# Kernel optimization log

Measured on AMD Instinct MI355X. Metric: run time of the kernel, lower is better.

## Reference

```python
import jax, jax.numpy as jnp
import numpy as np

# config constants (from init_kwargs)
MAX_WORD_LENGTH = 8
RESIDUAL_THRESHOLD = 1e-3
DECAY_FACTOR = 0.9


def setup_inputs() -> dict:
    key = jax.random.key(0)
    k1, k2 = jax.random.split(key)
    targets = jax.random.normal(k1, (8192, 1024), dtype=jnp.float32)
    codebook = jax.random.normal(k2, (4096, 1024), dtype=jnp.float32)
    return {"targets": targets, "codebook": codebook}


def reference(targets, codebook):
    """Batched greedy residual pursuit.

    targets:  [B, D] semantic vectors
    codebook: [K, D] syllable vectors
    Returns (indices [B, L] int32 with -1 where the per-sample loop broke,
             final residual [B, D]).
    """
    B = targets.shape[0]

    def step(carry, s):
        residual, active = carry  # [B, D], [B] bool
        # break condition checked BEFORE selecting, as in the torch loop
        norm = jnp.sqrt(jnp.sum(residual * residual, axis=-1))  # [B]
        active = active & (norm >= RESIDUAL_THRESHOLD)
        scores = jnp.einsum("bd,kd->bk", residual, codebook)  # [B, K]
        idx = jnp.argmax(scores, axis=-1)  # [B]
        decay = jnp.power(jnp.float32(DECAY_FACTOR), s.astype(jnp.float32))
        contribution = decay * codebook[idx]  # [B, D]
        residual = jnp.where(active[:, None], residual - contribution, residual)
        out_idx = jnp.where(active, idx, -1).astype(jnp.int32)
        return (residual, active), out_idx

    init = (targets, jnp.ones((B,), dtype=bool))
    (residual, _), idx_seq = jax.lax.scan(step, init, jnp.arange(MAX_WORD_LENGTH))
    indices = jnp.transpose(idx_seq)  # [B, L]
    return indices, residual
```

## Files before the change

### kernel.cpp

```cpp
#include <hip/hip_runtime.h>
#include <hip/hip_bf16.h>
#include <math.h>

#define NB 8192
#define NK 4096
#define ND 1024
#define NL 8
#define RES_THR 1e-3f

typedef __bf16 bf16x8 __attribute__((ext_vector_type(8)));
typedef float f32x4 __attribute__((ext_vector_type(4)));

#define MFMA16(a, b, c) __builtin_amdgcn_mfma_f32_16x16x32_bf16(a, b, c, 0, 0, 0)

#define GLOAD(g, l)                                                        \
  __builtin_amdgcn_global_load_lds(                                        \
      (const __attribute__((address_space(1))) void*)(g),                  \
      (__attribute__((address_space(3))) void*)(l), 16, 0, 0)

__device__ __forceinline__ unsigned short f2bf(float x) {
  __hip_bfloat16 h = __float2bfloat16(x);
  return __builtin_bit_cast(unsigned short, h);
}
__device__ __forceinline__ float bf2f(unsigned short u) {
  return __bfloat162float(__builtin_bit_cast(__hip_bfloat16, u));
}

__device__ __forceinline__ float wave_reduce_sum(float v) {
#pragma unroll
  for (int off = 32; off > 0; off >>= 1) v += __shfl_down(v, off);
  return v;
}

__device__ __forceinline__ void top2_merge(float& v1, int& k1, float& v2,
                                           int& k2, float w1, int j1, float w2,
                                           int j2) {
  if (w1 > v1 || (w1 == v1 && j1 < k1)) {
    if (v1 > w2 || (v1 == w2 && k1 < j2)) { v2 = v1; k2 = k1; }
    else { v2 = w2; k2 = j2; }
    v1 = w1; k1 = j1;
  } else {
    if (w1 > v2 || (w1 == v2 && j1 < k2)) { v2 = w1; k2 = j1; }
  }
}

__global__ __launch_bounds__(256) void k_prep(const float* __restrict__ cb,
                                              unsigned short* __restrict__ Bh) {
  int b = blockIdx.x, t = threadIdx.x;
  float4 v = ((const float4*)(cb + (size_t)b * ND))[t];
  ushort4 h;
  h.x = f2bf(v.x); h.y = f2bf(v.y); h.z = f2bf(v.z); h.w = f2bf(v.w);
  ((ushort4*)(Bh + (size_t)b * ND))[t] = h;
}

__global__ __launch_bounds__(256) void k_init(const float* __restrict__ tgt,
                                              float* __restrict__ resid,
                                              unsigned short* __restrict__ Ah,
                                              int* __restrict__ active) {
  int b = blockIdx.x, t = threadIdx.x;
  float4 v = ((const float4*)(tgt + (size_t)b * ND))[t];
  ((float4*)(resid + (size_t)b * ND))[t] = v;
  ushort4 h;
  h.x = f2bf(v.x); h.y = f2bf(v.y); h.z = f2bf(v.z); h.w = f2bf(v.w);
  ((ushort4*)(Ah + (size_t)b * ND))[t] = h;
  float ss = v.x * v.x + v.y * v.y + v.z * v.z + v.w * v.w;
  ss = wave_reduce_sum(ss);
  __shared__ float red[4];
  if ((t & 63) == 0) red[t >> 6] = ss;
  __syncthreads();
  if (t == 0) {
    float tot = red[0] + red[1] + red[2] + red[3];
    active[b] = (sqrtf(tot) >= RES_THR) ? 1 : 0;
  }
}

__global__ __launch_bounds__(512) void k_score0(
    const unsigned short* __restrict__ Ah, const unsigned short* __restrict__ Bh,
    float4* __restrict__ part, unsigned short* __restrict__ sc) {
  __shared__ __align__(16) char sA0[32768];
  __shared__ __align__(16) char sA1[32768];
  __shared__ __align__(16) char sB0[32768];
  __shared__ __align__(16) char sB1[32768];
  const int tid = threadIdx.x;
  const int lane = tid & 63;
  const int swzid = (blockIdx.x & 7) * 64 + (blockIdx.x >> 3);
  const int bm = swzid >> 4;
  const int bn = swzid & 15;
  const int wid = tid >> 6;
  const int wr = wid >> 2;
  const int wc = wid & 3;

  const int srow = tid >> 3;
  const int sblk = (tid & 7) ^ (srow & 7);
  const unsigned short* aSrc = Ah + (size_t)(bm * 256 + srow) * ND + sblk * 8;
  const unsigned short* bSrc = Bh + (size_t)(bn * 256 + srow) * ND + sblk * 8;

  const int lr = lane & 15;
  const int lk = lane >> 4;
  const int swz = lr & 7;
  const int kb0 = ((lk ^ swz) << 4);
  const int kb1 = (((4 + lk) ^ swz) << 4);

  f32x4 acc[8][4];
#pragma unroll
  for (int m = 0; m < 8; ++m)
#pragma unroll
    for (int n = 0; n < 4; ++n) acc[m][n] = (f32x4)(0.f);

#pragma unroll
  for (int rr = 0; rr < 4; ++rr) {
    GLOAD(aSrc + (size_t)(rr * 64) * ND, sA0 + rr * 8192 + tid * 16);
    GLOAD(bSrc + (size_t)(rr * 64) * ND, sB0 + rr * 8192 + tid * 16);
  }
#pragma unroll
  for (int rr = 0; rr < 4; ++rr) {
    GLOAD(aSrc + (size_t)(rr * 64) * ND + 64, sA1 + rr * 8192 + tid * 16);
    GLOAD(bSrc + (size_t)(rr * 64) * ND + 64, sB1 + rr * 8192 + tid * 16);
  }

#pragma unroll 1
  for (int kt = 0; kt < 16; ++kt) {
    const char* pa = (kt & 1) ? sA1 : sA0;
    const char* pb = (kt & 1) ? sB1 : sB0;
    if (kt < 15) {
      asm volatile("s_waitcnt vmcnt(8)" ::: "memory");
    } else {
      asm volatile("s_waitcnt vmcnt(0)" ::: "memory");
    }
    __builtin_amdgcn_s_barrier();
    bf16x8 af0[8], bf0[4];
#pragma unroll
    for (int m = 0; m < 8; ++m)
      af0[m] = *(const bf16x8*)(pa + (wr * 128 + m * 16 + lr) * 128 + kb0);
#pragma unroll
    for (int n = 0; n < 4; ++n)
      bf0[n] = *(const bf16x8*)(pb + (wc * 64 + n * 16 + lr) * 128 + kb0);
    __builtin_amdgcn_s_setprio(1);
#pragma unroll
    for (int m = 0; m < 8; ++m)
#pragma unroll
      for (int n = 0; n < 4; ++n) acc[m][n] = MFMA16(af0[m], bf0[n], acc[m][n]);
    __builtin_amdgcn_s_setprio(0);
    bf16x8 af1[8], bf1[4];
#pragma unroll
    for (int m = 0; m < 8; ++m)
      af1[m] = *(const bf16x8*)(pa + (wr * 128 + m * 16 + lr) * 128 + kb1);
#pragma unroll
    for (int n = 0; n < 4; ++n)
      bf1[n] = *(const bf16x8*)(pb + (wc * 64 + n * 16 + lr) * 128 + kb1);
    __syncthreads();
    if (kt < 14) {
      const int k0 = (kt + 2) << 6;
      char* da = (kt & 1) ? sA1 : sA0;
      char* db = (kt & 1) ? sB1 : sB0;
#pragma unroll
      for (int rr = 0; rr < 4; ++rr) {
        GLOAD(aSrc + (size_t)(rr * 64) * ND + k0, da + rr * 8192 + tid * 16);
        GLOAD(bSrc + (size_t)(rr * 64) * ND + k0, db + rr * 8192 + tid * 16);
      }
    }
    __builtin_amdgcn_s_setprio(1);
#pragma unroll
    for (int m = 0; m < 8; ++m)
#pragma unroll
      for (int n = 0; n < 4; ++n) acc[m][n] = MFMA16(af1[m], bf1[n], acc[m][n]);
    __builtin_amdgcn_s_setprio(0);
  }
  __syncthreads();

  if (sc) {
#pragma unroll
    for (int m = 0; m < 8; ++m) {
      int row = bm * 256 + wr * 128 + m * 16 + lk * 4;
#pragma unroll
      for (int q = 0; q < 4; ++q)
#pragma unroll
        for (int n = 0; n < 4; ++n)
          sc[(size_t)(row + q) * NK + bn * 256 + wc * 64 + n * 16 + lr] =
              f2bf(acc[m][n][q]);
    }
  }

  if (part) {
    float4* red = (float4*)sA0;
#pragma unroll
    for (int m = 0; m < 8; ++m) {
#pragma unroll
      for (int q = 0; q < 4; ++q) {
        float v1 = acc[m][0][q];
        int k1 = bn * 256 + wc * 64 + lr;
        float v2 = -INFINITY;
        int k2 = 0x7fffffff;
#pragma unroll
        for (int n = 1; n < 4; ++n) {
          top2_merge(v1, k1, v2, k2, acc[m][n][q],
                     bn * 256 + wc * 64 + n * 16 + lr, -INFINITY, 0x7fffffff);
        }
#pragma unroll
        for (int msk = 1; msk < 16; msk <<= 1) {
          float ov1 = __shfl_xor(v1, msk);
          int ok1 = __shfl_xor(k1, msk);
          float ov2 = __shfl_xor(v2, msk);
          int ok2 = __shfl_xor(k2, msk);
          top2_merge(v1, k1, v2, k2, ov1, ok1, ov2, ok2);
        }
        if (lr == 0) {
          int row = wr * 128 + m * 16 + lk * 4 + q;
          red[row * 4 + wc] =
              make_float4(v1, __int_as_float(k1), v2, __int_as_float(k2));
        }
      }
    }
    __syncthreads();
    if (tid < 256) {
      float4 e0 = red[tid * 4 + 0];
      float v1 = e0.x; int k1 = __float_as_int(e0.y);
      float v2 = e0.z; int k2 = __float_as_int(e0.w);
#pragma unroll
      for (int j = 1; j < 4; ++j) {
        float4 e = red[tid * 4 + j];
        top2_merge(v1, k1, v2, k2, e.x, __float_as_int(e.y), e.z,
                   __float_as_int(e.w));
      }
      part[(size_t)(bm * 256 + tid) * 16 + bn] =
          make_float4(v1, __int_as_float(k1), v2, __int_as_float(k2));
    }
  }
}

__global__ __launch_bounds__(512) void k_gram(const unsigned short* __restrict__ Bh,
                                              unsigned short* __restrict__ G) {
  __shared__ __align__(16) char sA0[32768];
  __shared__ __align__(16) char sA1[32768];
  __shared__ __align__(16) char sB0[32768];
  __shared__ __align__(16) char sB1[32768];
  const int tid = threadIdx.x;
  const int lane = tid & 63;
  const int bm = blockIdx.x >> 4;
  const int bn = blockIdx.x & 15;
  const int wid = tid >> 6;
  const int wr = wid >> 2;
  const int wc = wid & 3;
  const int srow = tid >> 3;
  const int sblk = (tid & 7) ^ (srow & 7);
  const unsigned short* aSrc = Bh + (size_t)(bm * 256 + srow) * ND + sblk * 8;
  const unsigned short* bSrc = Bh + (size_t)(bn * 256 + srow) * ND + sblk * 8;
  const int lr = lane & 15;
  const int lk = lane >> 4;
  const int swz = lr & 7;
  const int kb0 = ((lk ^ swz) << 4);
  const int kb1 = (((4 + lk) ^ swz) << 4);

  f32x4 acc[8][4];
#pragma unroll
  for (int m = 0; m < 8; ++m)
#pragma unroll
    for (int n = 0; n < 4; ++n) acc[m][n] = (f32x4)(0.f);

#pragma unroll
  for (int rr = 0; rr < 4; ++rr) {
    GLOAD(aSrc + (size_t)(rr * 64) * ND, sA0 + rr * 8192 + tid * 16);
    GLOAD(bSrc + (size_t)(rr * 64) * ND, sB0 + rr * 8192 + tid * 16);
  }
#pragma unroll
  for (int rr = 0; rr < 4; ++rr) {
    GLOAD(aSrc + (size_t)(rr * 64) * ND + 64, sA1 + rr * 8192 + tid * 16);
    GLOAD(bSrc + (size_t)(rr * 64) * ND + 64, sB1 + rr * 8192 + tid * 16);
  }
#pragma unroll 1
  for (int kt = 0; kt < 16; ++kt) {
    const char* pa = (kt & 1) ? sA1 : sA0;
    const char* pb = (kt & 1) ? sB1 : sB0;
    if (kt < 15) {
      asm volatile("s_waitcnt vmcnt(8)" ::: "memory");
    } else {
      asm volatile("s_waitcnt vmcnt(0)" ::: "memory");
    }
    __builtin_amdgcn_s_barrier();
    bf16x8 af0[8], bf0[4];
#pragma unroll
    for (int m = 0; m < 8; ++m)
      af0[m] = *(const bf16x8*)(pa + (wr * 128 + m * 16 + lr) * 128 + kb0);
#pragma unroll
    for (int n = 0; n < 4; ++n)
      bf0[n] = *(const bf16x8*)(pb + (wc * 64 + n * 16 + lr) * 128 + kb0);
    __builtin_amdgcn_s_setprio(1);
#pragma unroll
    for (int m = 0; m < 8; ++m)
#pragma unroll
      for (int n = 0; n < 4; ++n) acc[m][n] = MFMA16(af0[m], bf0[n], acc[m][n]);
    __builtin_amdgcn_s_setprio(0);
    bf16x8 af1[8], bf1[4];
#pragma unroll
    for (int m = 0; m < 8; ++m)
      af1[m] = *(const bf16x8*)(pa + (wr * 128 + m * 16 + lr) * 128 + kb1);
#pragma unroll
    for (int n = 0; n < 4; ++n)
      bf1[n] = *(const bf16x8*)(pb + (wc * 64 + n * 16 + lr) * 128 + kb1);
    __syncthreads();
    if (kt < 14) {
      const int k0 = (kt + 2) << 6;
      char* da = (kt & 1) ? sA1 : sA0;
      char* db = (kt & 1) ? sB1 : sB0;
#pragma unroll
      for (int rr = 0; rr < 4; ++rr) {
        GLOAD(aSrc + (size_t)(rr * 64) * ND + k0, da + rr * 8192 + tid * 16);
        GLOAD(bSrc + (size_t)(rr * 64) * ND + k0, db + rr * 8192 + tid * 16);
      }
    }
    __builtin_amdgcn_s_setprio(1);
#pragma unroll
    for (int m = 0; m < 8; ++m)
#pragma unroll
      for (int n = 0; n < 4; ++n) acc[m][n] = MFMA16(af1[m], bf1[n], acc[m][n]);
    __builtin_amdgcn_s_setprio(0);
  }
#pragma unroll
  for (int m = 0; m < 8; ++m) {
    int row = bm * 256 + wr * 128 + m * 16 + lk * 4;
#pragma unroll
    for (int q = 0; q < 4; ++q)
#pragma unroll
      for (int n = 0; n < 4; ++n)
        G[(size_t)(row + q) * NK + bn * 256 + wc * 64 + n * 16 + lr] =
            f2bf(acc[m][n][q]);
  }
}

__global__ __launch_bounds__(256) void k_all(
    const unsigned short* __restrict__ sc0, const unsigned short* __restrict__ G,
    const float* __restrict__ cb, float* __restrict__ resid,
    float* __restrict__ out_idx, const int* __restrict__ active0) {
  const int b = blockIdx.x, t = threadIdx.x;
  __shared__ float s_max[4];
  __shared__ float s_nrm[4];
  __shared__ float s_red[4];
  __shared__ int s_cnt;
  __shared__ int s_spec;
  __shared__ int s_k[64];
  __shared__ float s_bv;
  __shared__ int s_bk;

  float4 r = ((const float4*)(resid + (size_t)b * ND))[t];

  float scv[16];
  {
    const unsigned short* srow = sc0 + (size_t)b * NK;
    uint4 v0 = *(const uint4*)(srow + t * 8);
    uint4 v1 = *(const uint4*)(srow + 2048 + t * 8);
    unsigned w[8] = {v0.x, v0.y, v0.z, v0.w, v1.x, v1.y, v1.z, v1.w};
#pragma unroll
    for (int j = 0; j < 8; ++j) {
      scv[2 * j] = bf2f((unsigned short)(w[j] & 0xffff));
      scv[2 * j + 1] = bf2f((unsigned short)(w[j] >> 16));
    }
  }
  int act = active0[b];
  float decay = 1.0f;

#pragma unroll 1
  for (int s = 0; s < NL; ++s) {
    float m = scv[0];
#pragma unroll
    for (int i = 1; i < 16; ++i) m = fmaxf(m, scv[i]);
    float ss = r.x * r.x + r.y * r.y + r.z * r.z + r.w * r.w;
#pragma unroll
    for (int off = 32; off > 0; off >>= 1) {
      m = fmaxf(m, __shfl_xor(m, off));
      ss += __shfl_xor(ss, off);
    }
    if ((t & 63) == 0) { s_max[t >> 6] = m; s_nrm[t >> 6] = ss; }
    if (t == 0) {
      s_cnt = 0;
      s_spec = 0x7fffffff;
      s_bv = -INFINITY;
      s_bk = 0x7fffffff;
    }
    __syncthreads();
    const float M = fmaxf(fmaxf(s_max[0], s_max[1]), fmaxf(s_max[2], s_max[3]));
    const float nrm = s_nrm[0] + s_nrm[1] + s_nrm[2] + s_nrm[3];
    act = (act && sqrtf(nrm) >= RES_THR) ? 1 : 0;
    const float margin = (s == 0) ? 2.5f : 6.0f;
#pragma unroll
    for (int i = 0; i < 16; ++i) {
      if (scv[i] >= M - margin) {
        int col = (i < 8) ? (t * 8 + i) : (2048 + t * 8 + (i - 8));
        int pos = atomicAdd(&s_cnt, 1);
        if (pos < 64) s_k[pos] = col;
        if (scv[i] == M) atomicMin(&s_spec, col);
      }
    }
    __syncthreads();
    const int cnt = s_cnt < 64 ? s_cnt : 64;
    int kbest;
    if (cnt <= 1) {
      kbest = s_spec;
    } else {
      for (int c = 0; c < cnt; ++c) {
        int k = s_k[c];
        float4 cv = ((const float4*)(cb + (size_t)k * ND))[t];
        float dd = r.x * cv.x + r.y * cv.y + r.z * cv.z + r.w * cv.w;
        dd = wave_reduce_sum(dd);
        if ((t & 63) == 0) s_red[t >> 6] = dd;
        __syncthreads();
        if (t == 0) {
          float scr = s_red[0] + s_red[1] + s_red[2] + s_red[3];
          if (scr > s_bv || (scr == s_bv && k < s_bk)) { s_bv = scr; s_bk = k; }
        }
        __syncthreads();
      }
      kbest = s_bk;
    }
    if (t == 0) out_idx[(size_t)b * NL + s] = act ? (float)kbest : -1.0f;
    if (act) {
      float4 cv = ((const float4*)(cb + (size_t)kbest * ND))[t];
      r.x -= decay * cv.x;
      r.y -= decay * cv.y;
      r.z -= decay * cv.z;
      r.w -= decay * cv.w;
      if (s < NL - 1) {
        const unsigned short* grow = G + (size_t)kbest * NK;
        uint4 g0 = *(const uint4*)(grow + t * 8);
        uint4 g1 = *(const uint4*)(grow + 2048 + t * 8);
        unsigned w[8] = {g0.x, g0.y, g0.z, g0.w, g1.x, g1.y, g1.z, g1.w};
#pragma unroll
        for (int j = 0; j < 8; ++j) {
          scv[2 * j] -= decay * bf2f((unsigned short)(w[j] & 0xffff));
          scv[2 * j + 1] -= decay * bf2f((unsigned short)(w[j] >> 16));
        }
      }
    }
    decay *= 0.9f;
    __syncthreads();
  }
  ((float4*)(resid + (size_t)b * ND))[t] = r;
}

__global__ __launch_bounds__(256) void k_update(
    float* __restrict__ resid, const float* __restrict__ cb,
    const float4* __restrict__ part, int* __restrict__ active,
    float* __restrict__ out_idx, unsigned short* __restrict__ Ah, float decay,
    int s, int nseg, float margin) {
  int b = blockIdx.x, t = threadIdx.x;
  __shared__ int s_cnt;
  __shared__ int s_k[32];
  __shared__ float s_red[4];
  __shared__ float s_bv;
  __shared__ int s_bk;

  float4 r = ((const float4*)(resid + (size_t)b * ND))[t];

  if (t < 2 * nseg) {
    float4 e = part[(size_t)b * 16 + (t >> 1)];
    float v = (t & 1) ? e.z : e.x;
    int k = __float_as_int((t & 1) ? e.w : e.y);
    float M = v;
    for (int off = nseg; off > 0; off >>= 1) M = fmaxf(M, __shfl_xor(M, off));
    bool cand = (v >= M - margin);
    unsigned long long mask = __ballot(cand);
    int slot = __popcll(mask & ((1ull << t) - 1ull));
    if (cand && slot < 32) s_k[slot] = k;
    if (t == 0) {
      int n = (int)__popcll(mask);
      s_cnt = n < 32 ? n : 32;
      s_bv = -INFINITY;
      s_bk = 0x7fffffff;
    }
  }
  __syncthreads();
  int cnt = s_cnt;
  for (int c = 0; c < cnt; ++c) {
    int k = s_k[c];
    float4 cv = ((const float4*)(cb + (size_t)k * ND))[t];
    float dd = r.x * cv.x + r.y * cv.y + r.z * cv.z + r.w * cv.w;
    dd = wave_reduce_sum(dd);
    if ((t & 63) == 0) s_red[t >> 6] = dd;
    __syncthreads();
    if (t == 0) {
      float sc = s_red[0] + s_red[1] + s_red[2] + s_red[3];
      if (sc > s_bv || (sc == s_bv && k < s_bk)) { s_bv = sc; s_bk = k; }
    }
    __syncthreads();
  }
  int kbest = s_bk;
  int act = active[b];
  float4 cv = ((const float4*)(cb + (size_t)kbest * ND))[t];
  if (act) {
    r.x -= decay * cv.x;
    r.y -= decay * cv.y;
    r.z -= decay * cv.z;
    r.w -= decay * cv.w;
  }
  ((float4*)(resid + (size_t)b * ND))[t] = r;
  if (Ah) {
    ushort4 h;
    h.x = f2bf(r.x); h.y = f2bf(r.y); h.z = f2bf(r.z); h.w = f2bf(r.w);
    ((ushort4*)(Ah + (size_t)b * ND))[t] = h;
  }
  float ss = r.x * r.x + r.y * r.y + r.z * r.z + r.w * r.w;
  ss = wave_reduce_sum(ss);
  if ((t & 63) == 0) s_red[t >> 6] = ss;
  __syncthreads();
  if (t == 0) {
    float tot = s_red[0] + s_red[1] + s_red[2] + s_red[3];
    out_idx[(size_t)b * NL + s] = act ? (float)kbest : -1.0f;
    active[b] = (act && sqrtf(tot) >= RES_THR) ? 1 : 0;
  }
}

extern "C" void kernel_launch(void* const* d_in, const int* in_sizes, int n_in,
                              void* d_out, int out_size, void* d_ws,
                              size_t ws_size, hipStream_t stream) {
  const float* targets = (const float*)d_in[0];
  const float* codebook = (const float*)d_in[1];
  float* out = (float*)d_out;
  float* out_idx = out;
  float* resid = out + (size_t)NB * NL;

  char* ws = (char*)d_ws;
  const size_t SC_SZ = (size_t)NB * NK * 2;
  const size_t G_SZ = (size_t)NK * NK * 2;
  const size_t AH_SZ = (size_t)NB * ND * 2;
  const size_t BH_SZ = (size_t)NK * ND * 2;
  const size_t PART_SZ = (size_t)NB * 16 * 16;
  const size_t NEED = SC_SZ + G_SZ + AH_SZ + BH_SZ + PART_SZ + 32768;

  if (ws_size >= NEED) {
    unsigned short* scores = (unsigned short*)ws;
    unsigned short* G = (unsigned short*)(ws + SC_SZ);
    unsigned short* Ah = (unsigned short*)(ws + SC_SZ + G_SZ);
    unsigned short* Bh = (unsigned short*)(ws + SC_SZ + G_SZ + AH_SZ);
    int* active = (int*)(ws + SC_SZ + G_SZ + AH_SZ + BH_SZ + PART_SZ);

    k_prep<<<NK, 256, 0, stream>>>(codebook, Bh);
    k_init<<<NB, 256, 0, stream>>>(targets, resid, Ah, active);
    k_gram<<<256, 512, 0, stream>>>(Bh, G);
    k_score0<<<(NB / 256) * (NK / 256), 512, 0, stream>>>(Ah, Bh, nullptr,
                                                          scores);
    k_all<<<NB, 256, 0, stream>>>(scores, G, codebook, resid, out_idx, active);
  } else {
    float4* part = (float4*)ws;
    int* active = (int*)(ws + PART_SZ);
    unsigned short* Ah = (unsigned short*)(ws + PART_SZ + 65536);
    unsigned short* Bh = Ah + (size_t)NB * ND;

    k_prep<<<NK, 256, 0, stream>>>(codebook, Bh);
    k_init<<<NB, 256, 0, stream>>>(targets, resid, Ah, active);
    for (int s = 0; s < NL; ++s) {
      k_score0<<<(NB / 256) * (NK / 256), 512, 0, stream>>>(Ah, Bh, part,
                                                            nullptr);
      float ds = (float)pow(0.9, (double)s);
      k_update<<<NB, 256, 0, stream>>>(resid, codebook, part, active, out_idx,
                                       Ah, ds, s, 16, 2.5f);
    }
  }
}
```

Baseline: 274.1 us.

## Exploit Gram symmetry, merge prep kernels, drop fallback iterative path

The Gram matrix kernel now computes only the upper-triangular tiles (136 instead of 256 blocks) and writes each off-diagonal tile twice, once transposed, using the symmetry of codebook·codebookᵀ. The codebook and target conversion kernels are merged into one launch to save a kernel launch. The small-workspace fallback path, with its per-step scoring and update kernels, is removed. In exchange, the transposed stores are strided and uncoalesced, and the code now assumes the workspace is always large enough.

```diff
diff --git a/kernel.cpp b/kernel.cpp
--- a/kernel.cpp
+++ b/kernel.cpp
@@ -32,32 +32,21 @@
   return v;
 }
 
-__device__ __forceinline__ void top2_merge(float& v1, int& k1, float& v2,
-                                           int& k2, float w1, int j1, float w2,
-                                           int j2) {
-  if (w1 > v1 || (w1 == v1 && j1 < k1)) {
-    if (v1 > w2 || (v1 == w2 && k1 < j2)) { v2 = v1; k2 = k1; }
-    else { v2 = w2; k2 = j2; }
-    v1 = w1; k1 = j1;
-  } else {
-    if (w1 > v2 || (w1 == v2 && j1 < k2)) { v2 = w1; k2 = j1; }
-  }
-}
-
-__global__ __launch_bounds__(256) void k_prep(const float* __restrict__ cb,
-                                              unsigned short* __restrict__ Bh) {
+__global__ __launch_bounds__(256) void k_setup(const float* __restrict__ cb,
+                                               const float* __restrict__ tgt,
+                                               unsigned short* __restrict__ Bh,
+                                               float* __restrict__ resid,
+                                               unsigned short* __restrict__ Ah,
+                                               int* __restrict__ active) {
   int b = blockIdx.x, t = threadIdx.x;
-  float4 v = ((const float4*)(cb + (size_t)b * ND))[t];
-  ushort4 h;
-  h.x = f2bf(v.x); h.y = f2bf(v.y); h.z = f2bf(v.z); h.w = f2bf(v.w);
-  ((ushort4*)(Bh + (size_t)b * ND))[t] = h;
-}
-
-__global__ __launch_bounds__(256) void k_init(const float* __restrict__ tgt,
-                                              float* __restrict__ resid,
-                                              unsigned short* __restrict__ Ah,
-                                              int* __restrict__ active) {
-  int b = blockIdx.x, t = threadIdx.x;
+  if (b < NK) {
+    float4 v = ((const float4*)(cb + (size_t)b * ND))[t];
+    ushort4 h;
+    h.x = f2bf(v.x); h.y = f2bf(v.y); h.z = f2bf(v.z); h.w = f2bf(v.w);
+    ((ushort4*)(Bh + (size_t)b * ND))[t] = h;
+    return;
+  }
+  b -= NK;
   float4 v = ((const float4*)(tgt + (size_t)b * ND))[t];
   ((float4*)(resid + (size_t)b * ND))[t] = v;
   ushort4 h;
@@ -76,7 +65,7 @@
 
 __global__ __launch_bounds__(512) void k_score0(
     const unsigned short* __restrict__ Ah, const unsigned short* __restrict__ Bh,
-    float4* __restrict__ part, unsigned short* __restrict__ sc) {
+    unsigned short* __restrict__ sc) {
   __shared__ __align__(16) char sA0[32768];
   __shared__ __align__(16) char sA1[32768];
   __shared__ __align__(16) char sB0[32768];
@@ -168,63 +157,15 @@
   }
   __syncthreads();
 
-  if (sc) {
-#pragma unroll
-    for (int m = 0; m < 8; ++m) {
-      int row = bm * 256 + wr * 128 + m * 16 + lk * 4;
-#pragma unroll
-      for (int q = 0; q < 4; ++q)
-#pragma unroll
-        for (int n = 0; n < 4; ++n)
-          sc[(size_t)(row + q) * NK + bn * 256 + wc * 64 + n * 16 + lr] =
-              f2bf(acc[m][n][q]);
-    }
-  }
-
-  if (part) {
-    float4* red = (float4*)sA0;
-#pragma unroll
-    for (int m = 0; m < 8; ++m) {
-#pragma unroll
-      for (int q = 0; q < 4; ++q) {
-        float v1 = acc[m][0][q];
-        int k1 = bn * 256 + wc * 64 + lr;
-        float v2 = -INFINITY;
-        int k2 = 0x7fffffff;
-#pragma unroll
-        for (int n = 1; n < 4; ++n) {
-          top2_merge(v1, k1, v2, k2, acc[m][n][q],
-                     bn * 256 + wc * 64 + n * 16 + lr, -INFINITY, 0x7fffffff);
-        }
-#pragma unroll
-        for (int msk = 1; msk < 16; msk <<= 1) {
-          float ov1 = __shfl_xor(v1, msk);
-          int ok1 = __shfl_xor(k1, msk);
-          float ov2 = __shfl_xor(v2, msk);
-          int ok2 = __shfl_xor(k2, msk);
-          top2_merge(v1, k1, v2, k2, ov1, ok1, ov2, ok2);
-        }
-        if (lr == 0) {
-          int row = wr * 128 + m * 16 + lk * 4 + q;
-          red[row * 4 + wc] =
-              make_float4(v1, __int_as_float(k1), v2, __int_as_float(k2));
-        }
-      }
-    }
-    __syncthreads();
-    if (tid < 256) {
-      float4 e0 = red[tid * 4 + 0];
-      float v1 = e0.x; int k1 = __float_as_int(e0.y);
-      float v2 = e0.z; int k2 = __float_as_int(e0.w);
-#pragma unroll
-      for (int j = 1; j < 4; ++j) {
-        float4 e = red[tid * 4 + j];
-        top2_merge(v1, k1, v2, k2, e.x, __float_as_int(e.y), e.z,
-                   __float_as_int(e.w));
-      }
-      part[(size_t)(bm * 256 + tid) * 16 + bn] =
-          make_float4(v1, __int_as_float(k1), v2, __int_as_float(k2));
-    }
+#pragma unroll
+  for (int m = 0; m < 8; ++m) {
+    int row = bm * 256 + wr * 128 + m * 16 + lk * 4;
+#pragma unroll
+    for (int q = 0; q < 4; ++q)
+#pragma unroll
+      for (int n = 0; n < 4; ++n)
+        sc[(size_t)(row + q) * NK + bn * 256 + wc * 64 + n * 16 + lr] =
+            f2bf(acc[m][n][q]);
   }
 }
 
@@ -236,8 +177,9 @@
   __shared__ __align__(16) char sB1[32768];
   const int tid = threadIdx.x;
   const int lane = tid & 63;
-  const int bm = blockIdx.x >> 4;
-  const int bn = blockIdx.x & 15;
+  int bm = 0, rem = blockIdx.x;
+  while (rem >= 16 - bm) { rem -= 16 - bm; ++bm; }
+  const int bn = bm + rem;
   const int wid = tid >> 6;
   const int wr = wid >> 2;
   const int wc = wid & 3;
@@ -321,9 +263,12 @@
 #pragma unroll
     for (int q = 0; q < 4; ++q)
 #pragma unroll
-      for (int n = 0; n < 4; ++n)
-        G[(size_t)(row + q) * NK + bn * 256 + wc * 64 + n * 16 + lr] =
-            f2bf(acc[m][n][q]);
+      for (int n = 0; n < 4; ++n) {
+        int col = bn * 256 + wc * 64 + n * 16 + lr;
+        unsigned short v = f2bf(acc[m][n][q]);
+        G[(size_t)(row + q) * NK + col] = v;
+        if (bm != bn) G[(size_t)col * NK + (row + q)] = v;
+      }
   }
 }
 
@@ -436,78 +381,6 @@
   ((float4*)(resid + (size_t)b * ND))[t] = r;
 }
 
-__global__ __launch_bounds__(256) void k_update(
-    float* __restrict__ resid, const float* __restrict__ cb,
-    const float4* __restrict__ part, int* __restrict__ active,
-    float* __restrict__ out_idx, unsigned short* __restrict__ Ah, float decay,
-    int s, int nseg, float margin) {
-  int b = blockIdx.x, t = threadIdx.x;
-  __shared__ int s_cnt;
-  __shared__ int s_k[32];
-  __shared__ float s_red[4];
-  __shared__ float s_bv;
-  __shared__ int s_bk;
-
-  float4 r = ((const float4*)(resid + (size_t)b * ND))[t];
-
-  if (t < 2 * nseg) {
-    float4 e = part[(size_t)b * 16 + (t >> 1)];
-    float v = (t & 1) ? e.z : e.x;
-    int k = __float_as_int((t & 1) ? e.w : e.y);
-    float M = v;
-    for (int off = nseg; off > 0; off >>= 1) M = fmaxf(M, __shfl_xor(M, off));
-    bool cand = (v >= M - margin);
-    unsigned long long mask = __ballot(cand);
-    int slot = __popcll(mask & ((1ull << t) - 1ull));
-    if (cand && slot < 32) s_k[slot] = k;
-    if (t == 0) {
-      int n = (int)__popcll(mask);
-      s_cnt = n < 32 ? n : 32;
-      s_bv = -INFINITY;
-      s_bk = 0x7fffffff;
-    }
-  }
-  __syncthreads();
-  int cnt = s_cnt;
-  for (int c = 0; c < cnt; ++c) {
-    int k = s_k[c];
-    float4 cv = ((const float4*)(cb + (size_t)k * ND))[t];
-    float dd = r.x * cv.x + r.y * cv.y + r.z * cv.z + r.w * cv.w;
-    dd = wave_reduce_sum(dd);
-    if ((t & 63) == 0) s_red[t >> 6] = dd;
-    __syncthreads();
-    if (t == 0) {
-      float sc = s_red[0] + s_red[1] + s_red[2] + s_red[3];
-      if (sc > s_bv || (sc == s_bv && k < s_bk)) { s_bv = sc; s_bk = k; }
-    }
-    __syncthreads();
-  }
-  int kbest = s_bk;
-  int act = active[b];
-  float4 cv = ((const float4*)(cb + (size_t)kbest * ND))[t];
-  if (act) {
-    r.x -= decay * cv.x;
-    r.y -= decay * cv.y;
-    r.z -= decay * cv.z;
-    r.w -= decay * cv.w;
-  }
-  ((float4*)(resid + (size_t)b * ND))[t] = r;
-  if (Ah) {
-    ushort4 h;
-    h.x = f2bf(r.x); h.y = f2bf(r.y); h.z = f2bf(r.z); h.w = f2bf(r.w);
-    ((ushort4*)(Ah + (size_t)b * ND))[t] = h;
-  }
-  float ss = r.x * r.x + r.y * r.y + r.z * r.z + r.w * r.w;
-  ss = wave_reduce_sum(ss);
-  if ((t & 63) == 0) s_red[t >> 6] = ss;
-  __syncthreads();
-  if (t == 0) {
-    float tot = s_red[0] + s_red[1] + s_red[2] + s_red[3];
-    out_idx[(size_t)b * NL + s] = act ? (float)kbest : -1.0f;
-    active[b] = (act && sqrtf(tot) >= RES_THR) ? 1 : 0;
-  }
-}
-
 extern "C" void kernel_launch(void* const* d_in, const int* in_sizes, int n_in,
                               void* d_out, int out_size, void* d_ws,
                               size_t ws_size, hipStream_t stream) {
@@ -523,35 +396,16 @@
   const size_t AH_SZ = (size_t)NB * ND * 2;
   const size_t BH_SZ = (size_t)NK * ND * 2;
   const size_t PART_SZ = (size_t)NB * 16 * 16;
-  const size_t NEED = SC_SZ + G_SZ + AH_SZ + BH_SZ + PART_SZ + 32768;
-
-  if (ws_size >= NEED) {
-    unsigned short* scores = (unsigned short*)ws;
-    unsigned short* G = (unsigned short*)(ws + SC_SZ);
-    unsigned short* Ah = (unsigned short*)(ws + SC_SZ + G_SZ);
-    unsigned short* Bh = (unsigned short*)(ws + SC_SZ + G_SZ + AH_SZ);
-    int* active = (int*)(ws + SC_SZ + G_SZ + AH_SZ + BH_SZ + PART_SZ);
-
-    k_prep<<<NK, 256, 0, stream>>>(codebook, Bh);
-    k_init<<<NB, 256, 0, stream>>>(targets, resid, Ah, active);
-    k_gram<<<256, 512, 0, stream>>>(Bh, G);
-    k_score0<<<(NB / 256) * (NK / 256), 512, 0, stream>>>(Ah, Bh, nullptr,
-                                                          scores);
-    k_all<<<NB, 256, 0, stream>>>(scores, G, codebook, resid, out_idx, active);
-  } else {
-    float4* part = (float4*)ws;
-    int* active = (int*)(ws + PART_SZ);
-    unsigned short* Ah = (unsigned short*)(ws + PART_SZ + 65536);
-    unsigned short* Bh = Ah + (size_t)NB * ND;
-
-    k_prep<<<NK, 256, 0, stream>>>(codebook, Bh);
-    k_init<<<NB, 256, 0, stream>>>(targets, resid, Ah, active);
-    for (int s = 0; s < NL; ++s) {
-      k_score0<<<(NB / 256) * (NK / 256), 512, 0, stream>>>(Ah, Bh, part,
-                                                            nullptr);
-      float ds = (float)pow(0.9, (double)s);
-      k_update<<<NB, 256, 0, stream>>>(resid, codebook, part, active, out_idx,
-                                       Ah, ds, s, 16, 2.5f);
-    }
-  }
-}
+
+  unsigned short* scores = (unsigned short*)ws;
+  unsigned short* G = (unsigned short*)(ws + SC_SZ);
+  unsigned short* Ah = (unsigned short*)(ws + SC_SZ + G_SZ);
+  unsigned short* Bh = (unsigned short*)(ws + SC_SZ + G_SZ + AH_SZ);
+  int* active = (int*)(ws + SC_SZ + G_SZ + AH_SZ + BH_SZ + PART_SZ);
+
+  k_setup<<<NK + NB, 256, 0, stream>>>(codebook, targets, Bh, resid, Ah,
+                                       active);
+  k_gram<<<136, 512, 0, stream>>>(Bh, G);
+  k_score0<<<(NB / 256) * (NK / 256), 512, 0, stream>>>(Ah, Bh, scores);
+  k_all<<<NB, 256, 0, stream>>>(scores, G, codebook, resid, out_idx, active);
+}
```

Result: slower. 292.0 us (+6.5%).
